# Kernel tuning notes

Measured on AMD Instinct MI355X. Metric: run time of the kernel, lower is better.

## Reference

```python
import jax, jax.numpy as jnp
import numpy as np

H = 16            # num heads
D = 64            # head dim
HID = 1024        # hidden size
ALPHA = 1.0       # < 2 -> power-law kernel
BANDWIDTH = 1.0
A = 0.5           # doubly-stochastic exponent
RADIUS = 1.0      # sphere radius
EPS = 1e-7


def setup_inputs() -> dict:
    key = jax.random.key(0)
    ks = jax.random.split(key, 5)
    x = jax.random.normal(ks[0], (2, 2048, HID), dtype=jnp.float32)
    s = 1.0 / np.sqrt(HID)
    qkv_w = jax.random.normal(ks[1], (3 * HID, HID), dtype=jnp.float32) * s
    qkv_b = jnp.zeros((3 * HID,), dtype=jnp.float32)
    out_w = jax.random.normal(ks[2], (HID, HID), dtype=jnp.float32) * s
    out_b = jnp.zeros((HID,), dtype=jnp.float32)
    return {"x": x, "qkv_w": qkv_w, "qkv_b": qkv_b, "out_w": out_w, "out_b": out_b}


def _l2norm(t):
    # torch F.normalize(p=2, dim=-1): divide by max(||t||, 1e-12)
    n = jnp.sqrt(jnp.sum(t * t, axis=-1, keepdims=True))
    return t / jnp.maximum(n, 1e-12)


def reference(x, qkv_w, qkv_b, out_w, out_b):
    B, S, _ = x.shape
    qkv = x @ qkv_w.T + qkv_b                       # [B,S,3*HID]
    q, k, v = jnp.split(qkv, 3, axis=-1)
    # [B,H,S,D]
    q = _l2norm(q.reshape(B, S, H, D).transpose(0, 2, 1, 3))
    k = _l2norm(k.reshape(B, S, H, D).transpose(0, 2, 1, 3))
    v = v.reshape(B, S, H, D).transpose(0, 2, 1, 3)
    # geodesic distance on the sphere
    cos = jnp.clip(jnp.einsum('bhsd,bhtd->bhst', q, k), -1.0 + EPS, 1.0 - EPS)
    g_dist = jnp.arccos(cos) * RADIUS               # [B,H,S,S]
    # alpha < 2: power-law kernel
    attn_score = (1.0 + g_dist / jnp.sqrt(BANDWIDTH)) ** (-(D + ALPHA))
    # doubly-stochastic-style rescale: diag(row^-a) @ K @ diag(col^-a)
    row = attn_score.sum(-1) ** (-A)                # [B,H,S]
    col = attn_score.sum(-2) ** (-A)                # [B,H,S]
    k_tilde = row[..., :, None] * attn_score * col[..., None, :]
    # F.normalize(p=1, dim=3): divide by max(sum |.|, 1e-12); entries >= 0
    probs = k_tilde / jnp.maximum(k_tilde.sum(-1, keepdims=True), 1e-12)
    out = jnp.einsum('bhst,bhtd->bhsd', probs, v)   # [B,H,S,D]
    out = out.transpose(0, 2, 1, 3).reshape(B, S, HID)
    return out @ out_w.T + out_b
```

## Files before the change

### kernel.cpp

```cpp
#include <hip/hip_runtime.h>
#include <math.h>

#define NH   16
#define HD   64
#define HIDN 1024
#define NB   2
#define SEQ  2048
#define ROWS (NB*SEQ)
#define BH   (NB*NH)

typedef __attribute__((ext_vector_type(8))) short bf16x8;
typedef __attribute__((ext_vector_type(8))) _Float16 f16x8;
typedef __attribute__((ext_vector_type(4))) float f32x4;
typedef __attribute__((ext_vector_type(2))) float f32x2;
typedef _Float16 f16;

typedef const __attribute__((address_space(1))) void GV;
typedef __attribute__((address_space(3))) void LV;
__device__ __forceinline__ void glds16(const void* g, void* l) {
    __builtin_amdgcn_global_load_lds((GV*)g, (LV*)l, 16, 0, 0);
}

__device__ __forceinline__ unsigned short f2bf(float f) {
    unsigned u = __float_as_uint(f);
    u += 0x7FFF + ((u >> 16) & 1);
    return (unsigned short)(u >> 16);
}
__device__ __forceinline__ bf16x8 ldfrag(const unsigned short* p) {
    return *(const bf16x8*)p;
}
__device__ __forceinline__ f16x8 ldfragh(const f16* p) {
    return *(const f16x8*)p;
}
__device__ __forceinline__ f32x4 mfma16(bf16x8 a, bf16x8 b, f32x4 c) {
    return __builtin_amdgcn_mfma_f32_16x16x32_bf16(a, b, c, 0, 0, 0);
}
__device__ __forceinline__ f32x4 mfma16h(f16x8 a, f16x8 b, f32x4 c) {
    return __builtin_amdgcn_mfma_f32_16x16x32_f16(a, b, c, 0, 0, 0);
}

__device__ __forceinline__ f32x2 log2_1pacos_pair(float c0, float c1) {
    f32x2 u = { fmaxf(1.0f - c0, 0.0f), fmaxf(1.0f - c1, 0.0f) };
    f32x2 s = { __builtin_amdgcn_sqrtf(u.x), __builtin_amdgcn_sqrtf(u.y) };
    f32x2 p = u * 2.68532e-3f + 7.89259e-3f;
    p = u * p + 2.6516504e-2f;
    p = u * p + 1.1785113e-1f;
    p = u * p + 1.4142136f;
    f32x2 t = s * p + 1.0f;
    return (f32x2){ __builtin_amdgcn_logf(t.x), __builtin_amdgcn_logf(t.y) };
}
__device__ __forceinline__ unsigned packbf(f32x2 w) {
    return (__float_as_uint(w.x) >> 16) | (__float_as_uint(w.y) & 0xffff0000u);
}

__global__ __launch_bounds__(256)
void conv_f16(const float* __restrict__ src, f16* __restrict__ dst) {
    int i = (blockIdx.x * 256 + threadIdx.x) * 8;
    float4 a = *(const float4*)(src + i);
    float4 b = *(const float4*)(src + i + 4);
    f16x8 o = { (f16)a.x, (f16)a.y, (f16)a.z, (f16)a.w,
                (f16)b.x, (f16)b.y, (f16)b.z, (f16)b.w };
    *(f16x8*)(dst + i) = o;
}

__global__ __launch_bounds__(256)
void gemm_nt_f16(const f16* __restrict__ A, const f16* __restrict__ B,
                 const float* __restrict__ bias, float* __restrict__ C,
                 int M, int N, int K)
{
    __shared__ f16 As[128 * 32];
    __shared__ f16 Bs[128 * 32];
    const int tid = threadIdx.x;
    const int lane = tid & 63, w = tid >> 6;
    const int ln = lane & 15, lq = lane >> 4;
    const int wm = (w >> 1) * 64, wn = (w & 1) * 64;
    const int m0 = blockIdx.x * 128, n0 = blockIdx.y * 128;

    const int grow = lane >> 2;
    const int gcol = (lane & 3) * 8;
    const f16* Ab = A + (size_t)(m0 + w * 32 + grow) * K + gcol;
    const f16* Bb = B + (size_t)(n0 + w * 32 + grow) * K + gcol;
    f16* Asw = As + (w * 32) * 32;
    f16* Bsw = Bs + (w * 32) * 32;

    f32x4 acc[4][4];
    #pragma unroll
    for (int i = 0; i < 4; ++i)
        #pragma unroll
        for (int j = 0; j < 4; ++j) acc[i][j] = (f32x4){0.f, 0.f, 0.f, 0.f};

    for (int kc = 0; kc < K; kc += 32) {
        __syncthreads();
        #pragma unroll
        for (int i = 0; i < 2; ++i) {
            glds16(Ab + (size_t)(i * 16) * K + kc, Asw + (i * 16) * 32);
            glds16(Bb + (size_t)(i * 16) * K + kc, Bsw + (i * 16) * 32);
        }
        __syncthreads();
        f16x8 af[4], bf[4];
        #pragma unroll
        for (int i = 0; i < 4; ++i)
            af[i] = *(const f16x8*)&As[(wm + i * 16 + ln) * 32 + lq * 8];
        #pragma unroll
        for (int j = 0; j < 4; ++j)
            bf[j] = *(const f16x8*)&Bs[(wn + j * 16 + ln) * 32 + lq * 8];
        #pragma unroll
        for (int i = 0; i < 4; ++i)
            #pragma unroll
            for (int j = 0; j < 4; ++j)
                acc[i][j] = mfma16h(af[i], bf[j], acc[i][j]);
    }

    #pragma unroll
    for (int i = 0; i < 4; ++i) {
        #pragma unroll
        for (int j = 0; j < 4; ++j) {
            int colIdx = n0 + wn + j * 16 + ln;
            float bs = bias[colIdx];
            #pragma unroll
            for (int r = 0; r < 4; ++r) {
                int row = m0 + wm + i * 16 + lq * 4 + r;
                C[(size_t)row * N + colIdx] = acc[i][j][r] + bs;
            }
        }
    }
}

__global__ __launch_bounds__(256)
void normalize_qk_f16(const float* __restrict__ qkv,
                      f16* __restrict__ qf, f16* __restrict__ kf)
{
    int w    = blockIdx.x * 4 + (threadIdx.x >> 6);
    int lane = threadIdx.x & 63;
    int n = w >> 4, h = w & 15;
    int b = n >> 11, s = n & 2047;
    const float* base = qkv + (size_t)n * 3 * HIDN + h * HD;
    float q = base[lane], k = base[HIDN + lane];
    float qs = q * q, ks = k * k;
    #pragma unroll
    for (int o = 32; o; o >>= 1) { qs += __shfl_xor(qs, o); ks += __shfl_xor(ks, o); }
    q *= 1.0f / fmaxf(sqrtf(qs), 1e-12f);
    k *= 1.0f / fmaxf(sqrtf(ks), 1e-12f);
    size_t idx = ((size_t)((b * NH + h) * SEQ + s)) * HD + lane;
    qf[idx] = (f16)q;
    kf[idx] = (f16)k;
}

__global__ __launch_bounds__(256)
void v_transpose(const float* __restrict__ qkv, unsigned short* __restrict__ vth)
{
    __shared__ float Ls[64][65];
    int bh = blockIdx.y, s0 = blockIdx.x * 64;
    int b = bh >> 4, h = bh & 15;
    int tid = threadIdx.x;
    #pragma unroll
    for (int i = 0; i < 4; ++i) {
        int idx = tid + i * 256;
        int row = idx >> 4, c4 = (idx & 15) * 4;
        float4 v = *(const float4*)&qkv[((size_t)(b * SEQ + s0 + row)) * 3 * HIDN
                                        + 2 * HIDN + h * HD + c4];
        Ls[row][c4+0] = v.x; Ls[row][c4+1] = v.y; Ls[row][c4+2] = v.z; Ls[row][c4+3] = v.w;
    }
    __syncthreads();
    int d = tid >> 2, sb = (tid & 3) * 16;
    unsigned short hi[16];
    #pragma unroll
    for (int j = 0; j < 16; ++j) hi[j] = f2bf(Ls[sb + j][d]);
    size_t o = ((size_t)bh * HD + d) * SEQ + s0 + sb;
    *(uint4*)&vth[o]     = *(uint4*)&hi[0];
    *(uint4*)&vth[o + 8] = *(uint4*)&hi[8];
}

#define KSTR 72

__global__ __launch_bounds__(256)
void col_sum_f16(const f16* __restrict__ qf, const f16* __restrict__ kf,
                 float* __restrict__ colp)
{
    __shared__ __align__(16) f16 Qs[64 * KSTR];
    int bh = blockIdx.y;
    int tid = threadIdx.x, w = tid >> 6, lane = tid & 63, ln = lane & 15, lq = lane >> 4;
    int m0 = blockIdx.x * 128 + w * 32;
    const int st0 = blockIdx.z * (SEQ / 256);
    const f16* qb = qf + (size_t)bh * SEQ * HD;
    const int sr = tid >> 3;
    const int sc = (tid & 7) * 8;

    size_t rowK0 = ((size_t)bh * SEQ + m0 + ln) * HD;
    size_t rowK1 = ((size_t)bh * SEQ + m0 + 16 + ln) * HD;
    f16x8 kf0 = ldfragh(kf + rowK0 + lq * 8), kf1 = ldfragh(kf + rowK0 + 32 + lq * 8);
    f16x8 kf2 = ldfragh(kf + rowK1 + lq * 8), kf3 = ldfragh(kf + rowK1 + 32 + lq * 8);

    uint4 qa = *(const uint4*)(qb + (size_t)(st0 * 64 + sr) * HD + sc);
    uint4 qc = *(const uint4*)(qb + (size_t)(st0 * 64 + sr + 32) * HD + sc);

    f32x2 ca01 = {0.f, 0.f}, ca23 = {0.f, 0.f};
    f32x2 cb01 = {0.f, 0.f}, cb23 = {0.f, 0.f};
    #pragma unroll 1
    for (int st = st0; st < st0 + SEQ / 256; ++st) {
        __syncthreads();
        *(uint4*)&Qs[sr * KSTR + sc] = qa;
        *(uint4*)&Qs[(sr + 32) * KSTR + sc] = qc;
        int sn = (st + 1 < st0 + SEQ / 256) ? (st + 1) * 64 : st0 * 64;
        qa = *(const uint4*)(qb + (size_t)(sn + sr) * HD + sc);
        qc = *(const uint4*)(qb + (size_t)(sn + sr + 32) * HD + sc);
        __syncthreads();
        #pragma unroll
        for (int nt = 0; nt < 4; ++nt) {
            const f16* qp = &Qs[(nt * 16 + ln) * KSTR + lq * 8];
            f16x8 qfa = *(const f16x8*)qp, qfc = *(const f16x8*)(qp + 32);
            f32x4 s0 = {0.f, 0.f, 0.f, 0.f};
            s0 = mfma16h(kf0, qfa, s0);
            s0 = mfma16h(kf1, qfc, s0);
            f32x4 s1 = {0.f, 0.f, 0.f, 0.f};
            s1 = mfma16h(kf2, qfa, s1);
            s1 = mfma16h(kf3, qfc, s1);
            f32x2 la01 = log2_1pacos_pair(s0[0], s0[1]) * -65.0f;
            f32x2 la23 = log2_1pacos_pair(s0[2], s0[3]) * -65.0f;
            f32x2 lb01 = log2_1pacos_pair(s1[0], s1[1]) * -65.0f;
            f32x2 lb23 = log2_1pacos_pair(s1[2], s1[3]) * -65.0f;
            ca01 += (f32x2){ __builtin_amdgcn_exp2f(la01.x),
                             __builtin_amdgcn_exp2f(la01.y) };
            ca23 += (f32x2){ __builtin_amdgcn_exp2f(la23.x),
                             __builtin_amdgcn_exp2f(la23.y) };
            cb01 += (f32x2){ __builtin_amdgcn_exp2f(lb01.x),
                             __builtin_amdgcn_exp2f(lb01.y) };
            cb23 += (f32x2){ __builtin_amdgcn_exp2f(lb23.x),
                             __builtin_amdgcn_exp2f(lb23.y) };
        }
    }
    float cacc[2][4] = { {ca01.x, ca01.y, ca23.x, ca23.y},
                         {cb01.x, cb01.y, cb23.x, cb23.y} };
    #pragma unroll
    for (int hs = 0; hs < 2; ++hs) {
        #pragma unroll
        for (int r = 0; r < 4; ++r) {
            float v = cacc[hs][r];
            v += __shfl_xor(v, 1); v += __shfl_xor(v, 2);
            v += __shfl_xor(v, 4); v += __shfl_xor(v, 8);
            if (ln == 0)
                colp[(size_t)blockIdx.z * BH * SEQ + (size_t)bh * SEQ
                     + m0 + hs * 16 + lq * 4 + r] = v;
        }
    }
}

__global__ __launch_bounds__(256)
void col_finalize(const float* __restrict__ colp, float* __restrict__ col)
{
    int i = (blockIdx.x * 256 + threadIdx.x) * 4;
    float4 a = *(const float4*)&colp[i];
    float4 b = *(const float4*)&colp[(size_t)BH * SEQ + i];
    float4 c = *(const float4*)&colp[2 * (size_t)BH * SEQ + i];
    float4 d = *(const float4*)&colp[3 * (size_t)BH * SEQ + i];
    float4 o;
    o.x = -0.5f * __builtin_amdgcn_logf(a.x + b.x + c.x + d.x);
    o.y = -0.5f * __builtin_amdgcn_logf(a.y + b.y + c.y + d.y);
    o.z = -0.5f * __builtin_amdgcn_logf(a.z + b.z + c.z + d.z);
    o.w = -0.5f * __builtin_amdgcn_logf(a.w + b.w + c.w + d.w);
    *(float4*)&col[i] = o;
}

__global__ __launch_bounds__(256, 4)
void attn_f16(const f16* __restrict__ qf, const f16* __restrict__ kf,
              const unsigned short* __restrict__ vth,
              const float* __restrict__ col,
              float* __restrict__ numb, float* __restrict__ denb)
{
    __shared__ __align__(16) f16 Ks[64 * KSTR];
    __shared__ __align__(16) unsigned short Vs[64 * KSTR];
    __shared__ __align__(16) unsigned short Ws[4][32 * KSTR];
    __shared__ __align__(16) float lcls[64];
    int bh = blockIdx.y;
    int b = bh >> 4, h = bh & 15;
    int tid = threadIdx.x, w = tid >> 6, lane = tid & 63, ln = lane & 15, lq = lane >> 4;
    int m0 = blockIdx.x * 128 + w * 32;
    const int th = blockIdx.z;
    const int tb = th * (SEQ / 2);
    unsigned short* ws = Ws[w];

    const f16* kb = kf + (size_t)bh * SEQ * HD;
    const unsigned short* vb = vth + (size_t)bh * HD * SEQ;
    const float* cb = col + (size_t)bh * SEQ;

    const int sr = tid >> 3;
    const int sc = (tid & 7) * 8;

    size_t rowQ0 = ((size_t)bh * SEQ + m0 + ln) * HD;
    size_t rowQ1 = ((size_t)bh * SEQ + m0 + 16 + ln) * HD;
    f16x8 qf0 = ldfragh(qf + rowQ0 + lq * 8), qf1 = ldfragh(qf + rowQ0 + 32 + lq * 8);
    f16x8 qf2 = ldfragh(qf + rowQ1 + lq * 8), qf3 = ldfragh(qf + rowQ1 + 32 + lq * 8);

    bf16x8 ones;
    #pragma unroll
    for (int i = 0; i < 8; ++i) ones[i] = (short)0x3F80;

    f32x4 num[2][4];
    #pragma unroll
    for (int hs = 0; hs < 2; ++hs)
        #pragma unroll
        for (int nt = 0; nt < 4; ++nt) num[hs][nt] = (f32x4){0.f, 0.f, 0.f, 0.f};
    f32x4 den[2] = { {0.f, 0.f, 0.f, 0.f}, {0.f, 0.f, 0.f, 0.f} };

    uint4 ka = *(const uint4*)(kb + (size_t)(tb + sr) * HD + sc);
    uint4 kc = *(const uint4*)(kb + (size_t)(tb + sr + 32) * HD + sc);
    uint4 va = *(const uint4*)(vb + (size_t)sr * SEQ + tb + sc);
    uint4 vc = *(const uint4*)(vb + (size_t)(sr + 32) * SEQ + tb + sc);
    float clv = (tid < 64) ? cb[tb + tid] : 0.f;

    #pragma unroll 1
    for (int tt = 0; tt < SEQ / 128; ++tt) {
        __syncthreads();
        *(uint4*)&Ks[sr * KSTR + sc] = ka;
        *(uint4*)&Ks[(sr + 32) * KSTR + sc] = kc;
        *(uint4*)&Vs[sr * KSTR + sc] = va;
        *(uint4*)&Vs[(sr + 32) * KSTR + sc] = vc;
        if (tid < 64) lcls[tid] = clv;
        int tn = (tt + 1 < SEQ / 128) ? tb + (tt + 1) * 64 : tb;
        ka = *(const uint4*)(kb + (size_t)(tn + sr) * HD + sc);
        kc = *(const uint4*)(kb + (size_t)(tn + sr + 32) * HD + sc);
        va = *(const uint4*)(vb + (size_t)sr * SEQ + tn + sc);
        vc = *(const uint4*)(vb + (size_t)(sr + 32) * SEQ + tn + sc);
        clv = (tid < 64) ? cb[tn + tid] : 0.f;
        __syncthreads();

        #pragma unroll
        for (int nt = 0; nt < 4; ++nt) {
            const f16* kp = &Ks[(nt * 16 + ln) * KSTR + lq * 8];
            f16x8 kfa = *(const f16x8*)kp, kfc = *(const f16x8*)(kp + 32);
            float4 cl = *(const float4*)&lcls[nt * 16 + lq * 4];
            f32x4 s0 = {0.f, 0.f, 0.f, 0.f};
            s0 = mfma16h(kfa, qf0, s0);
            s0 = mfma16h(kfc, qf1, s0);
            f32x4 s1 = {0.f, 0.f, 0.f, 0.f};
            s1 = mfma16h(kfa, qf2, s1);
            s1 = mfma16h(kfc, qf3, s1);
            f32x2 a01 = log2_1pacos_pair(s0[0], s0[1]) * -65.0f + (f32x2){cl.x, cl.y};
            f32x2 a23 = log2_1pacos_pair(s0[2], s0[3]) * -65.0f + (f32x2){cl.z, cl.w};
            f32x2 b01 = log2_1pacos_pair(s1[0], s1[1]) * -65.0f + (f32x2){cl.x, cl.y};
            f32x2 b23 = log2_1pacos_pair(s1[2], s1[3]) * -65.0f + (f32x2){cl.z, cl.w};
            uint2 pw0, pw1;
            pw0.x = packbf((f32x2){ __builtin_amdgcn_exp2f(a01.x),
                                    __builtin_amdgcn_exp2f(a01.y) });
            pw0.y = packbf((f32x2){ __builtin_amdgcn_exp2f(a23.x),
                                    __builtin_amdgcn_exp2f(a23.y) });
            pw1.x = packbf((f32x2){ __builtin_amdgcn_exp2f(b01.x),
                                    __builtin_amdgcn_exp2f(b01.y) });
            pw1.y = packbf((f32x2){ __builtin_amdgcn_exp2f(b23.x),
                                    __builtin_amdgcn_exp2f(b23.y) });
            *(uint2*)(ws + ln * KSTR + nt * 16 + lq * 4) = pw0;
            *(uint2*)(ws + (16 + ln) * KSTR + nt * 16 + lq * 4) = pw1;
        }
        bf16x8 wa00 = ldfrag(ws + ln * KSTR + lq * 8);
        bf16x8 wa01 = ldfrag(ws + ln * KSTR + 32 + lq * 8);
        bf16x8 wa10 = ldfrag(ws + (16 + ln) * KSTR + lq * 8);
        bf16x8 wa11 = ldfrag(ws + (16 + ln) * KSTR + 32 + lq * 8);
        den[0] = mfma16(wa00, ones, den[0]);
        den[0] = mfma16(wa01, ones, den[0]);
        den[1] = mfma16(wa10, ones, den[1]);
        den[1] = mfma16(wa11, ones, den[1]);
        #pragma unroll
        for (int nt = 0; nt < 4; ++nt) {
            const unsigned short* vp = &Vs[(nt * 16 + ln) * KSTR + lq * 8];
            bf16x8 v0 = *(const bf16x8*)vp, v1 = *(const bf16x8*)(vp + 32);
            num[0][nt] = mfma16(wa00, v0, num[0][nt]);
            num[0][nt] = mfma16(wa01, v1, num[0][nt]);
            num[1][nt] = mfma16(wa10, v0, num[1][nt]);
            num[1][nt] = mfma16(wa11, v1, num[1][nt]);
        }
    }

    const size_t noff = (size_t)th * ROWS * HIDN;
    #pragma unroll
    for (int hs = 0; hs < 2; ++hs) {
        #pragma unroll
        for (int r = 0; r < 4; ++r) {
            int s = m0 + hs * 16 + lq * 4 + r;
            #pragma unroll
            for (int nt = 0; nt < 4; ++nt)
                numb[noff + ((size_t)(b * SEQ + s)) * HIDN + h * HD + nt * 16 + ln] =
                    num[hs][nt][r];
            if (ln == 0)
                denb[(size_t)th * BH * SEQ + (size_t)bh * SEQ + s] = den[hs][r];
        }
    }
}

__global__ __launch_bounds__(256)
void finalize_ctx(const float* __restrict__ numb, const float* __restrict__ denb,
                  f16* __restrict__ ctx)
{
    size_t i = ((size_t)blockIdx.x * 256 + threadIdx.x) * 8;
    int row = (int)(i >> 10);
    int cidx = (int)(i & (HIDN - 1));
    int b = row >> 11, s = row & 2047;
    int h = cidx >> 6;
    size_t di = (size_t)(b * NH + h) * SEQ + s;
    float d = denb[di] + denb[(size_t)BH * SEQ + di];
    float inv = 1.0f / fmaxf(d, 1e-12f);
    const float* n1 = numb + (size_t)ROWS * HIDN;
    float4 a0 = *(const float4*)&numb[i];
    float4 a1 = *(const float4*)&numb[i + 4];
    float4 b0 = *(const float4*)&n1[i];
    float4 b1 = *(const float4*)&n1[i + 4];
    f16x8 o = { (f16)((a0.x + b0.x) * inv), (f16)((a0.y + b0.y) * inv),
                (f16)((a0.z + b0.z) * inv), (f16)((a0.w + b0.w) * inv),
                (f16)((a1.x + b1.x) * inv), (f16)((a1.y + b1.y) * inv),
                (f16)((a1.z + b1.z) * inv), (f16)((a1.w + b1.w) * inv) };
    *(f16x8*)(ctx + i) = o;
}

extern "C" void kernel_launch(void* const* d_in, const int* in_sizes, int n_in,
                              void* d_out, int out_size, void* d_ws, size_t ws_size,
                              hipStream_t stream) {
    const float* x      = (const float*)d_in[0];
    const float* qkv_w  = (const float*)d_in[1];
    const float* qkv_b  = (const float*)d_in[2];
    const float* out_w  = (const float*)d_in[3];
    const float* out_b  = (const float*)d_in[4];
    float* out = (float*)d_out;

    const size_t NTT = (size_t)BH * SEQ * HD;
    float* qkv = (float*)d_ws;
    float* colp = qkv;
    float* denb = qkv + 4 * (size_t)BH * SEQ;
    float* numb = qkv + 6 * (size_t)BH * SEQ;
    float* col = qkv + (size_t)ROWS * 3 * HIDN;
    f16* xh    = (f16*)(col + (size_t)BH * SEQ);
    f16* wqh   = xh + (size_t)ROWS * HIDN;
    f16* woh   = wqh + (size_t)3 * HIDN * HIDN;
    f16* ctxh  = woh + (size_t)HIDN * HIDN;
    f16* qfp   = ctxh + (size_t)ROWS * HIDN;
    f16* kfp   = qfp + NTT;
    unsigned short* vth = (unsigned short*)(kfp + NTT);

    conv_f16<<<ROWS*HIDN/2048, 256, 0, stream>>>(x, xh);
    conv_f16<<<3*HIDN*HIDN/2048, 256, 0, stream>>>(qkv_w, wqh);
    conv_f16<<<HIDN*HIDN/2048, 256, 0, stream>>>(out_w, woh);

    gemm_nt_f16<<<dim3(ROWS/128, 3*HIDN/128), 256, 0, stream>>>(
        xh, wqh, qkv_b, qkv, ROWS, 3*HIDN, HIDN);
    normalize_qk_f16<<<ROWS*NH/4, 256, 0, stream>>>(qkv, qfp, kfp);
    v_transpose<<<dim3(SEQ/64, BH), 256, 0, stream>>>(qkv, vth);
    col_sum_f16<<<dim3(SEQ/128, BH, 4), 256, 0, stream>>>(qfp, kfp, colp);
    col_finalize<<<BH*SEQ/1024, 256, 0, stream>>>(colp, col);
    attn_f16<<<dim3(SEQ/128, BH, 2), 256, 0, stream>>>(qfp, kfp, vth, col,
                                                       numb, denb);
    finalize_ctx<<<ROWS*HIDN/2048, 256, 0, stream>>>(numb, denb, ctxh);
    gemm_nt_f16<<<dim3(ROWS/128, HIDN/128), 256, 0, stream>>>(
        ctxh, woh, out_b, out, ROWS, HIDN, HIDN);
}
```

Measured before the change: 316.0 us.

## Feed attention weights straight from registers into K16 MFMAs, dropping LDS staging

The kernel previously wrote the bf16 attention weights into a per-wave shared-memory buffer and reloaded them as 16x16x32 MFMA A-fragments. It now uses the output layout of the score MFMA directly as the A operand of 16x16x16 bf16 MFMAs, issued per 16-key sub-tile inside the score loop. This removes the LDS write/read round trip and frees the Ws shared memory. The cost is twice as many (smaller) MFMA instructions and narrower 8-byte V fragment loads from LDS.

```diff
diff --git a/kernel.cpp b/kernel.cpp
--- a/kernel.cpp
+++ b/kernel.cpp
@@ -10,6 +10,7 @@
 #define BH   (NB*NH)
 
 typedef __attribute__((ext_vector_type(8))) short bf16x8;
+typedef __attribute__((ext_vector_type(4))) short bf16x4;
 typedef __attribute__((ext_vector_type(8))) _Float16 f16x8;
 typedef __attribute__((ext_vector_type(4))) float f32x4;
 typedef __attribute__((ext_vector_type(2))) float f32x2;
@@ -37,6 +38,9 @@
 }
 __device__ __forceinline__ f32x4 mfma16h(f16x8 a, f16x8 b, f32x4 c) {
     return __builtin_amdgcn_mfma_f32_16x16x32_f16(a, b, c, 0, 0, 0);
+}
+__device__ __forceinline__ f32x4 mfma16k16(bf16x4 a, bf16x4 b, f32x4 c) {
+    return __builtin_amdgcn_mfma_f32_16x16x16bf16_1k(a, b, c, 0, 0, 0);
 }
 
 __device__ __forceinline__ f32x2 log2_1pacos_pair(float c0, float c1) {
@@ -269,7 +273,6 @@
 {
     __shared__ __align__(16) f16 Ks[64 * KSTR];
     __shared__ __align__(16) unsigned short Vs[64 * KSTR];
-    __shared__ __align__(16) unsigned short Ws[4][32 * KSTR];
     __shared__ __align__(16) float lcls[64];
     int bh = blockIdx.y;
     int b = bh >> 4, h = bh & 15;
@@ -277,7 +280,6 @@
     int m0 = blockIdx.x * 128 + w * 32;
     const int th = blockIdx.z;
     const int tb = th * (SEQ / 2);
-    unsigned short* ws = Ws[w];
 
     const f16* kb = kf + (size_t)bh * SEQ * HD;
     const unsigned short* vb = vth + (size_t)bh * HD * SEQ;
@@ -291,15 +293,15 @@
     f16x8 qf0 = ldfragh(qf + rowQ0 + lq * 8), qf1 = ldfragh(qf + rowQ0 + 32 + lq * 8);
     f16x8 qf2 = ldfragh(qf + rowQ1 + lq * 8), qf3 = ldfragh(qf + rowQ1 + 32 + lq * 8);
 
-    bf16x8 ones;
-    #pragma unroll
-    for (int i = 0; i < 8; ++i) ones[i] = (short)0x3F80;
+    bf16x4 ones4;
+    #pragma unroll
+    for (int i = 0; i < 4; ++i) ones4[i] = (short)0x3F80;
 
     f32x4 num[2][4];
     #pragma unroll
     for (int hs = 0; hs < 2; ++hs)
         #pragma unroll
-        for (int nt = 0; nt < 4; ++nt) num[hs][nt] = (f32x4){0.f, 0.f, 0.f, 0.f};
+        for (int nd = 0; nd < 4; ++nd) num[hs][nd] = (f32x4){0.f, 0.f, 0.f, 0.f};
     f32x4 den[2] = { {0.f, 0.f, 0.f, 0.f}, {0.f, 0.f, 0.f, 0.f} };
 
     uint4 ka = *(const uint4*)(kb + (size_t)(tb + sr) * HD + sc);
@@ -348,25 +350,19 @@
                                     __builtin_amdgcn_exp2f(b01.y) });
             pw1.y = packbf((f32x2){ __builtin_amdgcn_exp2f(b23.x),
                                     __builtin_amdgcn_exp2f(b23.y) });
-            *(uint2*)(ws + ln * KSTR + nt * 16 + lq * 4) = pw0;
-            *(uint2*)(ws + (16 + ln) * KSTR + nt * 16 + lq * 4) = pw1;
-        }
-        bf16x8 wa00 = ldfrag(ws + ln * KSTR + lq * 8);
-        bf16x8 wa01 = ldfrag(ws + ln * KSTR + 32 + lq * 8);
-        bf16x8 wa10 = ldfrag(ws + (16 + ln) * KSTR + lq * 8);
-        bf16x8 wa11 = ldfrag(ws + (16 + ln) * KSTR + 32 + lq * 8);
-        den[0] = mfma16(wa00, ones, den[0]);
-        den[0] = mfma16(wa01, ones, den[0]);
-        den[1] = mfma16(wa10, ones, den[1]);
-        den[1] = mfma16(wa11, ones, den[1]);
-        #pragma unroll
-        for (int nt = 0; nt < 4; ++nt) {
-            const unsigned short* vp = &Vs[(nt * 16 + ln) * KSTR + lq * 8];
-            bf16x8 v0 = *(const bf16x8*)vp, v1 = *(const bf16x8*)(vp + 32);
-            num[0][nt] = mfma16(wa00, v0, num[0][nt]);
-            num[0][nt] = mfma16(wa01, v1, num[0][nt]);
-            num[1][nt] = mfma16(wa10, v0, num[1][nt]);
-            num[1][nt] = mfma16(wa11, v1, num[1][nt]);
+            bf16x4 wf0 = *(const bf16x4*)&pw0;
+            bf16x4 wf1 = *(const bf16x4*)&pw1;
+            bf16x4 vf[4];
+            #pragma unroll
+            for (int nd = 0; nd < 4; ++nd)
+                vf[nd] = *(const bf16x4*)&Vs[(nd * 16 + ln) * KSTR + nt * 16 + lq * 4];
+            den[0] = mfma16k16(wf0, ones4, den[0]);
+            den[1] = mfma16k16(wf1, ones4, den[1]);
+            #pragma unroll
+            for (int nd = 0; nd < 4; ++nd) {
+                num[0][nd] = mfma16k16(wf0, vf[nd], num[0][nd]);
+                num[1][nd] = mfma16k16(wf1, vf[nd], num[1][nd]);
+            }
         }
     }
 
@@ -377,9 +373,9 @@
         for (int r = 0; r < 4; ++r) {
             int s = m0 + hs * 16 + lq * 4 + r;
             #pragma unroll
-            for (int nt = 0; nt < 4; ++nt)
-                numb[noff + ((size_t)(b * SEQ + s)) * HIDN + h * HD + nt * 16 + ln] =
-                    num[hs][nt][r];
+            for (int nd = 0; nd < 4; ++nd)
+                numb[noff + ((size_t)(b * SEQ + s)) * HIDN + h * HD + nd * 16 + ln] =
+                    num[hs][nd][r];
             if (ln == 0)
                 denb[(size_t)th * BH * SEQ + (size_t)bh * SEQ + s] = den[hs][r];
         }
```

New measurement: 320.6 us. No clear change (+1.5%).
